# Kernel optimization log

Measured on AMD Instinct MI355X. Metric: run time of the kernel, lower is better.

Reference implementation:

```python
import jax, jax.numpy as jnp
import numpy as np
from jax import lax

B, T_IN, T_OUT = 32, 256, 500
N_MEL, ENC_DIM = 80, 512
ATT_RNN, DEC_RNN, PRENET, ATT_DIM = 1024, 1024, 256, 128
LOC_F, LOC_K = 32, 31
P_ATT_DROP, P_DEC_DROP = 0.1, 0.1


def setup_inputs() -> dict:
    key = jax.random.key(0)
    ks = jax.random.split(key, 24)
    rn = lambda k, s, sc=0.02: jax.random.normal(k, s, dtype=jnp.float32) * sc
    inp = {}
    inp['memory'] = jax.random.normal(ks[0], (B, T_IN, ENC_DIM), dtype=jnp.float32)
    inp['decoder_inputs'] = jax.random.normal(ks[1], (B, N_MEL, T_OUT), dtype=jnp.float32)
    inp['memory_lengths'] = jax.random.randint(ks[2], (B,), T_IN // 2, T_IN + 1)
    inp['prenet_w1'] = rn(ks[3], (PRENET, N_MEL))
    inp['prenet_w2'] = rn(ks[4], (PRENET, PRENET))
    inp['att_w_ih'] = rn(ks[5], (4 * ATT_RNN, PRENET + ENC_DIM))
    inp['att_w_hh'] = rn(ks[6], (4 * ATT_RNN, ATT_RNN))
    inp['att_b_ih'] = jnp.zeros((4 * ATT_RNN,), jnp.float32)
    inp['att_b_hh'] = jnp.zeros((4 * ATT_RNN,), jnp.float32)
    inp['query_w'] = rn(ks[7], (ATT_DIM, ATT_RNN))
    inp['memory_w'] = rn(ks[8], (ATT_DIM, ENC_DIM))
    inp['v_w'] = rn(ks[9], (1, ATT_DIM))
    inp['loc_conv_w'] = rn(ks[10], (LOC_F, 2, LOC_K))
    inp['loc_dense_w'] = rn(ks[11], (ATT_DIM, LOC_F))
    inp['dec_w_ih'] = rn(ks[12], (4 * DEC_RNN, ATT_RNN + ENC_DIM))
    inp['dec_w_hh'] = rn(ks[13], (4 * DEC_RNN, DEC_RNN))
    inp['dec_b_ih'] = jnp.zeros((4 * DEC_RNN,), jnp.float32)
    inp['dec_b_hh'] = jnp.zeros((4 * DEC_RNN,), jnp.float32)
    inp['proj_w'] = rn(ks[14], (N_MEL, DEC_RNN + ENC_DIM))
    inp['proj_b'] = jnp.zeros((N_MEL,), jnp.float32)
    inp['gate_w'] = rn(ks[15], (1, DEC_RNN + ENC_DIM))
    inp['gate_b'] = jnp.zeros((1,), jnp.float32)
    return inp


def _lstm_cell(x, h, c, w_ih, w_hh, b_ih, b_hh):
    gates = x @ w_ih.T + b_ih + h @ w_hh.T + b_hh
    i, f, g, o = jnp.split(gates, 4, axis=-1)
    c2 = jax.nn.sigmoid(f) * c + jax.nn.sigmoid(i) * jnp.tanh(g)
    h2 = jax.nn.sigmoid(o) * jnp.tanh(c2)
    return h2, c2


def _dropout_masks():
    # deterministic dropout masks (training=True semantics), keep-prob scaled
    kd = jax.random.key(1)
    k1, k2, k3, k4 = jax.random.split(kd, 4)
    m1 = jax.random.bernoulli(k1, 0.5, (T_OUT + 1, B, PRENET)).astype(jnp.float32) / 0.5
    m2 = jax.random.bernoulli(k2, 0.5, (T_OUT + 1, B, PRENET)).astype(jnp.float32) / 0.5
    ma = jax.random.bernoulli(k3, 1 - P_ATT_DROP, (T_OUT, B, ATT_RNN)).astype(jnp.float32) / (1 - P_ATT_DROP)
    md = jax.random.bernoulli(k4, 1 - P_DEC_DROP, (T_OUT, B, DEC_RNN)).astype(jnp.float32) / (1 - P_DEC_DROP)
    return m1, m2, ma, md


def _decode(memory, decoder_inputs, memory_lengths, prenet_w1, prenet_w2,
            att_w_ih, att_w_hh, att_b_ih, att_b_hh, query_w, memory_w, v_w,
            loc_conv_w, loc_dense_w, dec_w_ih, dec_w_hh, dec_b_ih, dec_b_hh,
            proj_w, proj_b, gate_w, gate_b):
    pm1, pm2, att_drop, dec_drop = _dropout_masks()
    processed_memory = jnp.einsum('bte,ae->bta', memory, memory_w)  # (B,T_in,128)
    pad_mask = jnp.arange(T_IN)[None, :] >= memory_lengths[:, None]  # True = padded

    # teacher-forced decoder inputs: (B,n_mel,T) -> (T,B,n_mel), prepend go frame
    dec_in = jnp.transpose(decoder_inputs, (2, 0, 1))
    dec_in = jnp.concatenate([jnp.zeros((1, B, N_MEL), dec_in.dtype), dec_in], 0)
    # prenet (relu + dropout p=0.5, always training)
    x = jax.nn.relu(dec_in @ prenet_w1.T) * pm1
    x = jax.nn.relu(x @ prenet_w2.T) * pm2
    prenet_out = x[:T_OUT]  # (T,B,256)

    pad = (LOC_K - 1) // 2

    def attention(att_h, aw, aw_cum):
        pq = att_h @ query_w.T  # (B,128)
        awc = jnp.stack([aw, aw_cum], axis=1)  # (B,2,T_in)
        loc = lax.conv_general_dilated(awc, loc_conv_w, (1,), [(pad, pad)],
                                       dimension_numbers=('NCH', 'OIH', 'NCH'))  # (B,32,T_in)
        loc = jnp.einsum('bft,af->bta', loc, loc_dense_w)  # (B,T_in,128)
        energies = jnp.tanh(pq[:, None, :] + loc + processed_memory) @ v_w[0]  # (B,T_in)
        energies = jnp.where(pad_mask, -jnp.inf, energies)
        w = jax.nn.softmax(energies, axis=1)
        ctx = jnp.einsum('bt,bte->be', w, memory)  # (B,512)
        return ctx, w

    def step(carry, xs):
        ah, ac, dh, dc, aw, aw_cum, ctx = carry
        pn, adm, ddm = xs
        cell_in = jnp.concatenate([pn, ctx], axis=-1)  # (B,768)
        ah, ac = _lstm_cell(cell_in, ah, ac, att_w_ih, att_w_hh, att_b_ih, att_b_hh)
        ah = ah * adm
        ctx, aw = attention(ah, aw, aw_cum)
        aw_cum = aw_cum + aw
        din = jnp.concatenate([ah, ctx], axis=-1)  # (B,1536)
        dh, dc = _lstm_cell(din, dh, dc, dec_w_ih, dec_w_hh, dec_b_ih, dec_b_hh)
        dh = dh * ddm
        dhac = jnp.concatenate([dh, ctx], axis=-1)  # (B,1536)
        mel = dhac @ proj_w.T + proj_b  # (B,80)
        gate = (dhac @ gate_w.T + gate_b)[:, 0]  # (B,)
        return (ah, ac, dh, dc, aw, aw_cum, ctx), (mel, gate, aw)

    z = lambda d: jnp.zeros((B, d), jnp.float32)
    init = (z(ATT_RNN), z(ATT_RNN), z(DEC_RNN), z(DEC_RNN),
            jnp.zeros((B, T_IN), jnp.float32), jnp.zeros((B, T_IN), jnp.float32), z(ENC_DIM))
    _, (mels, gates, aligns) = lax.scan(step, init, (prenet_out, att_drop, dec_drop))

    mel_outputs = jnp.transpose(mels, (1, 2, 0))   # (B, n_mel, T_out)
    gate_outputs = gates.T                          # (B, T_out)
    alignments = jnp.transpose(aligns, (1, 0, 2))   # (B, T_out, T_in)
    return mel_outputs, gate_outputs, alignments


def reference(memory, decoder_inputs, memory_lengths, prenet_w1, prenet_w2,
              att_w_ih, att_w_hh, att_b_ih, att_b_hh, query_w, memory_w, v_w,
              loc_conv_w, loc_dense_w, dec_w_ih, dec_w_hh, dec_b_ih, dec_b_hh,
              proj_w, proj_b, gate_w, gate_b):
    return _decode(memory, decoder_inputs, memory_lengths, prenet_w1, prenet_w2,
                   att_w_ih, att_w_hh, att_b_ih, att_b_hh, query_w, memory_w, v_w,
                   loc_conv_w, loc_dense_w, dec_w_ih, dec_w_hh, dec_b_ih, dec_b_hh,
                   proj_w, proj_b, gate_w, gate_b)
```

## Files before the change

kernel.cpp:

```cpp
#include <hip/hip_runtime.h>
#include <math.h>
#include <string.h>

#define TOUT 500
#define AOFF 1296000
#define GOFF 1280000
#define TF_BITS_XOR 1

typedef float f32x4 __attribute__((ext_vector_type(4)));
typedef short bf16x8 __attribute__((ext_vector_type(8)));
typedef unsigned short ushort4_t __attribute__((ext_vector_type(4)));
typedef unsigned u32x4 __attribute__((ext_vector_type(4)));

struct Params {
  const float *memory, *dec_in, *pw1, *pw2, *awih, *awhh, *abih, *abhh;
  const float *qw, *mw, *vw, *lcw, *ldw, *dwih, *dwhh, *dbih, *dbhh;
  const float *pjw, *pjb, *gw, *gb;
  const int* mlen;
  float* out;
  unsigned short *ahb0, *ahb1, *dhb0, *dhb1, *ctxb0, *ctxb1;
  unsigned *barcl;
  unsigned *barcr;
  unsigned *barg;
  float *x1, *w1t, *w2t, *mwt, *ldwt, *ba, *bd;
  unsigned short *pre_bf, *pm_bf, *mem_bf, *qw_bf, *wpa, *wpd;
  unsigned *mma, *mmd, *mm1, *mm2;
};

__host__ __device__ inline void tf_block(unsigned k0, unsigned k1, unsigned x0, unsigned x1,
                                         unsigned& o0, unsigned& o1) {
  unsigned ks2 = k0 ^ k1 ^ 0x1BD11BDAu;
  x0 += k0; x1 += k1;
#define TFR(r) { x0 += x1; x1 = (x1 << r) | (x1 >> (32 - r)); x1 ^= x0; }
  TFR(13) TFR(15) TFR(26) TFR(6)
  x0 += k1;  x1 += ks2 + 1u;
  TFR(17) TFR(29) TFR(16) TFR(24)
  x0 += ks2; x1 += k0 + 2u;
  TFR(13) TFR(15) TFR(26) TFR(6)
  x0 += k0;  x1 += k1 + 3u;
  TFR(17) TFR(29) TFR(16) TFR(24)
  x0 += k1;  x1 += ks2 + 4u;
  TFR(13) TFR(15) TFR(26) TFR(6)
  x0 += ks2; x1 += k0 + 5u;
#undef TFR
  o0 = x0; o1 = x1;
}

__device__ inline float sigf(float x) { return 1.f / (1.f + __expf(-x)); }
__device__ inline float tanh_fast(float x) {
  float ax = fabsf(x);
  float t = __expf(-2.f * ax);
  float r = (1.f - t) / (1.f + t);
  return copysignf(r, x);
}
__device__ inline unsigned short f2bf(float f) {
  unsigned u = __float_as_uint(f);
  unsigned r = (u + 0x7FFFu + ((u >> 16) & 1u)) >> 16;
  return (unsigned short)r;
}
__device__ inline float bf2f(unsigned short u) {
  return __uint_as_float((unsigned)u << 16);
}

__device__ inline unsigned long long ld_coh64(const void* ptr) {
  return __hip_atomic_load((unsigned long long*)ptr, __ATOMIC_RELAXED, __HIP_MEMORY_SCOPE_SYSTEM);
}
__device__ inline void st_coh32(unsigned* ptr, unsigned v) {
  __hip_atomic_store(ptr, v, __ATOMIC_RELAXED, __HIP_MEMORY_SCOPE_SYSTEM);
}

template<bool COH>
__device__ __forceinline__ u32x4 ld16(const void* ptr) {
  u32x4 r;
  if constexpr (COH)
    asm volatile("global_load_dwordx4 %0, %1, off sc0 sc1" : "=v"(r) : "v"(ptr));
  else
    asm volatile("global_load_dwordx4 %0, %1, off" : "=v"(r) : "v"(ptr));
  return r;
}

#define LD4(p) (*(const float4*)(p))

__global__ void maskgen_kernel(Params p, unsigned k1a, unsigned k1b, unsigned k2a, unsigned k2b,
                               unsigned k3a, unsigned k3b, unsigned k4a, unsigned k4b) {
  int t = blockIdx.x * 256 + threadIdx.x;
  unsigned ka, kb; unsigned* dst; float pp;
  if (t < 512000)       { ka = k3a; kb = k3b; dst = p.mma; pp = 0.9f; }
  else if (t < 1024000) { t -= 512000;  ka = k4a; kb = k4b; dst = p.mmd; pp = 0.9f; }
  else if (t < 1152256) { t -= 1024000; ka = k1a; kb = k1b; dst = p.mm1; pp = 0.5f; }
  else if (t < 1280512) { t -= 1152256; ka = k2a; kb = k2b; dst = p.mm2; pp = 0.5f; }
  else return;
  unsigned word = 0u;
  for (int i = 0; i < 32; ++i) {
    unsigned o0, o1;
    tf_block(ka, kb, 0u, (unsigned)t * 32u + (unsigned)i, o0, o1);
#if TF_BITS_XOR
    unsigned bits = o0 ^ o1;
#else
    unsigned bits = o0;
#endif
    unsigned fb = (bits >> 9) | 0x3f800000u;
    float u = __uint_as_float(fb) - 1.0f;
    if (u < pp) word |= (1u << i);
  }
  dst[t] = word;
}

__global__ void prep_misc(Params p) {
  int i = blockIdx.x * 256 + threadIdx.x;
  if (i < 20480) { int k = i >> 8, u = i & 255; p.w1t[i] = p.pw1[u * 80 + k]; return; }
  i -= 20480;
  if (i < 65536) { int k = i >> 8, u = i & 255; p.w2t[i] = p.pw2[u * 256 + k]; return; }
  i -= 65536;
  if (i < 65536) { int k = i >> 7, a = i & 127; p.mwt[i] = p.mw[a * 512 + k]; return; }
  i -= 65536;
  if (i < 131072) { p.qw_bf[i] = f2bf(p.qw[i]); return; }
  i -= 131072;
  if (i < 4096) { int f = i >> 7, a = i & 127; p.ldwt[i] = p.ldw[a * 32 + f]; return; }
  i -= 4096;
  if (i < 4096) { int col = (i & 3) * 1024 + (i >> 2); p.ba[i] = p.abih[col] + p.abhh[col]; return; }
  i -= 4096;
  if (i < 4096) { int col = (i & 3) * 1024 + (i >> 2); p.bd[i] = p.dbih[col] + p.dbhh[col]; return; }
  i -= 4096;
  if (i < 4194304) { p.mem_bf[i] = f2bf(p.memory[i]); return; }
}

__global__ void pack_att(Params p) {
  int idx = blockIdx.x * 256 + threadIdx.x;
  if (idx >= 256 * 56 * 64) return;
  int l = idx & 63;
  int c = (idx >> 6) % 56;
  int T = idx / (56 * 64);
  int n = T * 16 + (l & 15);
  int col = (n & 3) * 1024 + (n >> 2);
  int kb = c * 32 + 8 * (l >> 4);
  bf16x8 v;
#pragma unroll
  for (int j = 0; j < 8; ++j) {
    int k = kb + j;
    float f = (k < 768) ? p.awih[(size_t)col * 768 + k] : p.awhh[(size_t)col * 1024 + k - 768];
    v[j] = (short)f2bf(f);
  }
  *(bf16x8*)(p.wpa + (size_t)idx * 8) = v;
}
__global__ void pack_dec(Params p) {
  int idx = blockIdx.x * 256 + threadIdx.x;
  if (idx >= 256 * 80 * 64) return;
  int l = idx & 63;
  int c = (idx >> 6) % 80;
  int T = idx / (80 * 64);
  int n = T * 16 + (l & 15);
  int col = (n & 3) * 1024 + (n >> 2);
  int kb = c * 32 + 8 * (l >> 4);
  bf16x8 v;
#pragma unroll
  for (int j = 0; j < 8; ++j) {
    int k = kb + j;
    float f = (k < 1536) ? p.dwih[(size_t)col * 1536 + k] : p.dwhh[(size_t)col * 1024 + k - 1536];
    v[j] = (short)f2bf(f);
  }
  *(bf16x8*)(p.wpd + (size_t)idx * 8) = v;
}

__global__ void prenet1_kernel(Params p) {
  __shared__ float din[8][80];
  int wg = blockIdx.x, tid = threadIdx.x;
  int r0 = wg * 8;
  for (int idx = tid; idx < 8 * 80; idx += 256) {
    int j = idx / 80, kk = idx % 80;
    int r = r0 + j; int t = r >> 5, b = r & 31;
    din[j][kk] = (t == 0) ? 0.f : p.dec_in[(size_t)b * 40000 + (size_t)kk * 500 + (t - 1)];
  }
  __syncthreads();
  float acc[8] = {0,0,0,0,0,0,0,0};
  for (int k = 0; k < 80; ++k) {
    float wv = p.w1t[k * 256 + tid];
#pragma unroll
    for (int j = 0; j < 8; ++j) acc[j] += din[j][k] * wv;
  }
  for (int j = 0; j < 8; ++j) {
    int r = r0 + j;
    unsigned e = (unsigned)r * 256u + tid;
    float mv = ((p.mm1[e >> 5] >> (e & 31)) & 1u) ? 2.0f : 0.0f;
    p.x1[(size_t)r * 256 + tid] = fmaxf(acc[j], 0.f) * mv;
  }
}
__global__ void prenet2_kernel(Params p) {
  __shared__ float rows[8][256];
  int wg = blockIdx.x, tid = threadIdx.x;
  int r0 = wg * 8;
  for (int idx = tid; idx < 8 * 256; idx += 256) {
    int j = idx >> 8, kk = idx & 255;
    rows[j][kk] = p.x1[(size_t)(r0 + j) * 256 + kk];
  }
  __syncthreads();
  float acc[8] = {0,0,0,0,0,0,0,0};
  for (int k = 0; k < 256; ++k) {
    float wv = p.w2t[k * 256 + tid];
#pragma unroll
    for (int j = 0; j < 8; ++j) acc[j] += rows[j][k] * wv;
  }
  for (int j = 0; j < 8; ++j) {
    int r = r0 + j;
    unsigned e = (unsigned)r * 256u + tid;
    float mv = ((p.mm2[e >> 5] >> (e & 31)) & 1u) ? 2.0f : 0.0f;
    p.pre_bf[(size_t)r * 256 + tid] = f2bf(fmaxf(acc[j], 0.f) * mv);
  }
}

__global__ void pm_kernel(Params p) {
  __shared__ float mrows[16][512];
  int wg = blockIdx.x;
  int b = wg >> 4, tc = wg & 15;
  int tid = threadIdx.x;
  int t0 = tc * 16;
  for (int idx = tid; idx < 16 * 512; idx += 128) {
    int i = idx >> 9, k = idx & 511;
    mrows[i][k] = p.memory[((size_t)b * 256 + t0 + i) * 512 + k];
  }
  __syncthreads();
  float acc[16];
#pragma unroll
  for (int i = 0; i < 16; ++i) acc[i] = 0.f;
  for (int k = 0; k < 512; ++k) {
    float wv = p.mwt[k * 128 + tid];
#pragma unroll
    for (int i = 0; i < 16; ++i) acc[i] += mrows[i][k] * wv;
  }
  for (int i = 0; i < 16; ++i)
    p.pm_bf[((size_t)b * 256 + t0 + i) * 128 + tid] = f2bf(acc[i]);
}

template<int LEN, bool COH>
struct Seg {
  static constexpr int CPR = LEN / 8;
  static constexpr int N = (32 * CPR) / 512;
  u32x4 r[N];
  __device__ __forceinline__ void load(const unsigned short* src, int srcStride, int tid) {
#pragma unroll
    for (int i = 0; i < N; ++i) {
      int idx = tid + i * 512;
      int b = idx / CPR, c = idx % CPR;
      r[i] = ld16<COH>(src + (size_t)b * srcStride + c * 8);
    }
  }
  __device__ __forceinline__ void store(unsigned short* dst, int dstOff, int dstStride, int tid) {
#pragma unroll
    for (int i = 0; i < N; ++i) {
      int idx = tid + i * 512;
      int b = idx / CPR, c = idx % CPR;
      *(u32x4*)(dst + b * dstStride + dstOff + c * 8) = r[i];
    }
  }
};

__device__ __forceinline__ void drain_vm() {
  asm volatile("s_waitcnt vmcnt(0)" ::: "memory");
  __builtin_amdgcn_sched_barrier(0);
}

#define MFMA_BF16(a, b, c) __builtin_amdgcn_mfma_f32_16x16x32_bf16(a, b, c, 0, 0, 0)

template<int NC, int CPW, int P0J, bool ATT>
__device__ __forceinline__ void gemm_tile2(const Params& p, const bf16x8* bfa, const bf16x8* bfb,
                                           int lane, int v, int s,
                                           const unsigned short* ctxb_prev,
                                           const unsigned short* ahb_prev,
                                           const unsigned short* dhb_prev2,
                                           unsigned short* Abuf, float* pl, int tid) {
  const int arow = lane & 15;
  const int kgrp = (lane >> 4) * 8;
  f32x4 acc00 = {0,0,0,0}, acc01 = {0,0,0,0}, acc10 = {0,0,0,0}, acc11 = {0,0,0,0};

  const int RS0 = ATT ? 776 : 1288;
  if (ATT) {
    Seg<256, false> s0; Seg<512, true> s1;
    s0.load(p.pre_bf + (size_t)s * 32 * 256, 256, tid);
    s1.load(ctxb_prev, 512, tid);
    drain_vm();
    s0.store(Abuf, 0, RS0, tid);
    s1.store(Abuf, 256, RS0, tid);
  } else {
    Seg<1024, true> s0; Seg<256, true> s1;
    s0.load(ahb_prev, 1024, tid);
    s1.load(ctxb_prev, 512, tid);
    drain_vm();
    s0.store(Abuf, 0, RS0, tid);
    s1.store(Abuf, 1024, RS0, tid);
  }
  __syncthreads();
#pragma unroll
  for (int j = 0; j < P0J; ++j) {
    const int kc = (v + 8 * j) * 32;
    const int off = arow * RS0 + kc + kgrp;
    bf16x8 a0 = *(const bf16x8*)&Abuf[off];
    bf16x8 a1 = *(const bf16x8*)&Abuf[off + 16 * RS0];
    acc00 = MFMA_BF16(a0, bfa[j], acc00);
    acc01 = MFMA_BF16(a1, bfa[j], acc01);
    acc10 = MFMA_BF16(a0, bfb[j], acc10);
    acc11 = MFMA_BF16(a1, bfb[j], acc11);
  }
  __syncthreads();

  const int RS1 = ATT ? 1032 : 1288;
  if (ATT) {
    Seg<1024, true> s0;
    s0.load(ahb_prev, 1024, tid);
    drain_vm();
    s0.store(Abuf, 0, RS1, tid);
  } else {
    Seg<256, true> s0; Seg<1024, true> s1;
    s0.load(ctxb_prev + 256, 512, tid);
    s1.load(dhb_prev2, 1024, tid);
    drain_vm();
    s0.store(Abuf, 0, RS1, tid);
    s1.store(Abuf, 256, RS1, tid);
  }
  __syncthreads();
  const int K1 = ATT ? 768 : 1280;
#pragma unroll
  for (int j = P0J; j < CPW; ++j) {
    const int kc = (v + 8 * j) * 32 - K1;
    const int off = arow * RS1 + kc + kgrp;
    bf16x8 a0 = *(const bf16x8*)&Abuf[off];
    bf16x8 a1 = *(const bf16x8*)&Abuf[off + 16 * RS1];
    acc00 = MFMA_BF16(a0, bfa[j], acc00);
    acc01 = MFMA_BF16(a1, bfa[j], acc01);
    acc10 = MFMA_BF16(a0, bfb[j], acc10);
    acc11 = MFMA_BF16(a1, bfb[j], acc11);
  }
  __syncthreads();

  const int po = (lane & 15) * 17 + (lane >> 4) * 4;
#pragma unroll
  for (int j = 0; j < 4; ++j) {
    pl[v * 1088 +   0 + po + j] = acc00[j];
    pl[v * 1088 + 272 + po + j] = acc01[j];
    pl[v * 1088 + 544 + po + j] = acc10[j];
    pl[v * 1088 + 816 + po + j] = acc11[j];
  }
}

template<bool IS_ATT>
__device__ __forceinline__ void run_scan(const Params& p, int wg, int tid,
                                         unsigned short* Abuf, float* pl, float* gates,
                                         float* cst, float* aw_l, float* awc_l, float* sm,
                                         unsigned short* ahst, unsigned short* cxst,
                                         unsigned short* hst) {
  const int lane = tid & 63;
  const int v = tid >> 6;
  constexpr int NC  = IS_ATT ? 56 : 80;
  constexpr int CPW = IS_ATT ? 7 : 10;
  constexpr int P0J = IS_ATT ? 3 : 5;
  const int wgl = IS_ATT ? wg : (wg - 128);
  const int Tb  = wgl * 2;
  const int grp = wg >> 5;
  const int pollIdx = (wg & 7) * 32;

  bf16x8 bfa[CPW], bfb[CPW];
  {
    const unsigned short* wp = IS_ATT ? p.wpa : p.wpd;
#pragma unroll
    for (int j = 0; j < CPW; ++j) {
      const int c = v + 8 * j;
      const unsigned short* bp = wp + ((size_t)(Tb * NC + c) * 64 + lane) * 8;
      bfa[j] = *(const bf16x8*)bp;
      bfb[j] = *(const bf16x8*)(bp + (size_t)NC * 64 * 8);
    }
  }

  unsigned bargen = 0;
  auto gbar = [&]() {
    ++bargen;
    __syncthreads();
    if (tid == 0) {
      const int pr = bargen & 1;
      unsigned old = __hip_atomic_fetch_add(p.barcl + (pr * 8 + grp) * 32, 1u,
                                            __ATOMIC_RELAXED, __HIP_MEMORY_SCOPE_SYSTEM);
      bool done = false;
      if (old == 31u) {
        unsigned old2 = __hip_atomic_fetch_add(p.barcr + pr * 32, 1u,
                                               __ATOMIC_RELAXED, __HIP_MEMORY_SCOPE_SYSTEM);
        if (old2 == 7u) {
#pragma unroll
          for (int i = 0; i < 8; ++i)
            __hip_atomic_store(p.barcl + (pr * 8 + i) * 32, 0u, __ATOMIC_RELAXED, __HIP_MEMORY_SCOPE_SYSTEM);
          __hip_atomic_store(p.barcr + pr * 32, 0u, __ATOMIC_RELAXED, __HIP_MEMORY_SCOPE_SYSTEM);
          asm volatile("s_waitcnt vmcnt(0)" ::: "memory");
#pragma unroll
          for (int i = 0; i < 8; ++i)
            __hip_atomic_store(p.barg + i * 32, bargen, __ATOMIC_RELAXED, __HIP_MEMORY_SCOPE_SYSTEM);
          done = true;
        }
      }
      if (!done) {
        while (__hip_atomic_load(p.barg + pollIdx, __ATOMIC_RELAXED, __HIP_MEMORY_SCOPE_SYSTEM) < bargen)
          __builtin_amdgcn_s_sleep(2);
      }
    }
    __syncthreads();
  };

  for (int s = 0; s <= 500; ++s) {
    const int sb = s & 1;
    const unsigned short* ahb_prev  = sb ? p.ahb0 : p.ahb1;
    unsigned short*       ahb_cur   = sb ? p.ahb1 : p.ahb0;
    const unsigned short* dhb_prev2 = sb ? p.dhb1 : p.dhb0;
    unsigned short*       dhb_out   = sb ? p.dhb0 : p.dhb1;
    const unsigned short* ctxb_prev = sb ? p.ctxb0 : p.ctxb1;
    unsigned short*       ctxb_cur  = sb ? p.ctxb1 : p.ctxb0;

    const bool gemm_on = IS_ATT ? (s < 500) : (s >= 1);

    if (gemm_on)
      gemm_tile2<NC, CPW, P0J, IS_ATT>(p, bfa, bfb, lane, v, s, ctxb_prev, ahb_prev, dhb_prev2, Abuf, pl, tid);
    __syncthreads();
    if (gemm_on) {
      const float* bias = IS_ATT ? p.ba : p.bd;
      const int nb32 = wgl * 32;
#pragma unroll
      for (int rep = 0; rep < 2; ++rep) {
        int o = rep * 512 + tid;
        int tile = o >> 9, half = (o >> 8) & 1, n = (o >> 4) & 15, brow = o & 15;
        int o2 = (tile * 2 + half) * 272 + n * 17 + brow;
        float acc = 0.f;
#pragma unroll
        for (int w = 0; w < 8; ++w) acc += pl[w * 1088 + o2];
        int n_local = tile * 16 + n;
        gates[n_local * 33 + half * 16 + brow] = acc + bias[nb32 + n_local];
      }
    }
    __syncthreads();
    if (gemm_on && tid < 256) {
      int u_local = tid >> 5, b = tid & 31;
      float gi = gates[(u_local * 4 + 0) * 33 + b];
      float gf = gates[(u_local * 4 + 1) * 33 + b];
      float gg = gates[(u_local * 4 + 2) * 33 + b];
      float go = gates[(u_local * 4 + 3) * 33 + b];
      float I = sigf(gi), F = sigf(gf), G = tanh_fast(gg), O = sigf(go);
      float c2 = F * cst[tid] + I * G;
      float h = O * tanh_fast(c2);
      cst[tid] = c2;
      int u = wgl * 8 + u_local;
      float mv;
      if (IS_ATT) {
        unsigned e = ((unsigned)s * 32 + b) * 1024u + u;
        mv = ((p.mma[e >> 5] >> (e & 31)) & 1u) ? (1.f / 0.9f) : 0.f;
      } else {
        unsigned e = ((unsigned)(s - 1) * 32 + b) * 1024u + u;
        mv = ((p.mmd[e >> 5] >> (e & 31)) & 1u) ? (1.f / 0.9f) : 0.f;
      }
      hst[tid] = f2bf(h * mv);
    }
    __syncthreads();
    if (gemm_on && tid < 128) {
      int j = tid >> 5, bb = tid & 31;
      unsigned lo = hst[j * 64 + bb], hi = hst[j * 64 + 32 + bb];
      unsigned val = lo | (hi << 16);
      unsigned short* basep = IS_ATT ? ahb_cur : dhb_out;
      int T8 = wgl * 8;
      st_coh32((unsigned*)(basep + (size_t)bb * 1024 + T8 + 2 * j), val);
    }

    gbar();

    if (IS_ATT && wg < 32) {
      if (s < 500) {
        const int b = wg;
        unsigned short* locT_bf = (unsigned short*)pl;
        float* ldwt_l = (float*)((char*)(void*)pl + 16640);
        {
          const float4* srcw = (const float4*)p.ldwt;
          float4* dstw = (float4*)ldwt_l;
          dstw[tid] = srcw[tid];
          dstw[tid + 512] = srcw[tid + 512];
        }
        if (tid < 256) {
          unsigned long long q = ld_coh64((const unsigned long long*)(ahb_cur + (size_t)b * 1024) + tid);
          *(unsigned long long*)&ahst[tid * 4] = q;
        }
#pragma unroll
        for (int rep = 0; rep < 4; ++rep) {
          int qd = rep * 512 + tid;
          int f = qd >> 6, tq = (qd & 63) * 4;
          const float* wf = p.lcw + f * 62;
          float w[36]; float acc[4] = {0, 0, 0, 0};
#pragma unroll
          for (int j2 = 0; j2 < 9; ++j2) {
            float4 x = *(const float4*)&aw_l[tq + j2 * 4];
            w[j2*4] = x.x; w[j2*4+1] = x.y; w[j2*4+2] = x.z; w[j2*4+3] = x.w;
          }
#pragma unroll
          for (int k = 0; k < 31; ++k) {
            float cc = wf[k];
            acc[0] += w[k+1]*cc; acc[1] += w[k+2]*cc; acc[2] += w[k+3]*cc; acc[3] += w[k+4]*cc;
          }
#pragma unroll
          for (int j2 = 0; j2 < 9; ++j2) {
            float4 x = *(const float4*)&awc_l[tq + j2 * 4];
            w[j2*4] = x.x; w[j2*4+1] = x.y; w[j2*4+2] = x.z; w[j2*4+3] = x.w;
          }
#pragma unroll
          for (int k = 0; k < 31; ++k) {
            float cc = wf[31 + k];
            acc[0] += w[k+1]*cc; acc[1] += w[k+2]*cc; acc[2] += w[k+3]*cc; acc[3] += w[k+4]*cc;
          }
#pragma unroll
          for (int j2 = 0; j2 < 4; ++j2) locT_bf[f * 260 + tq + j2] = f2bf(acc[j2]);
        }
        __syncthreads();
        {
          int a = tid & 127, kq = tid >> 7;
          const unsigned short* qp = p.qw_bf + (size_t)a * 1024 + kq * 256;
          float acc = 0.f;
#pragma unroll 4
          for (int j = 0; j < 256; j += 8) {
            bf16x8 qv = *(const bf16x8*)(qp + j);
            bf16x8 av = *(const bf16x8*)&ahst[kq * 256 + j];
#pragma unroll
            for (int j2 = 0; j2 < 8; ++j2)
              acc += bf2f((unsigned short)av[j2]) * bf2f((unsigned short)qv[j2]);
          }
          sm[256 + kq * 128 + a] = acc;
          if (tid < 128) sm[128 + tid] = p.vw[tid];
        }
        __syncthreads();
        if (tid < 128) sm[tid] = sm[256 + tid] + sm[384 + tid] + sm[512 + tid] + sm[640 + tid];
        __syncthreads();
        {
          int t = tid & 255, h2 = tid >> 8;
          float lt[32];
#pragma unroll
          for (int f = 0; f < 32; ++f) lt[f] = bf2f(locT_bf[f * 260 + t]);
          const unsigned short* pmp = p.pm_bf + ((size_t)b * 256 + t) * 128;
          float e = 0.f;
#pragma unroll 2
          for (int ac = 0; ac < 16; ++ac) {
            int a0 = h2 * 64 + ac * 4;
            float4 l2 = {0, 0, 0, 0};
#pragma unroll
            for (int f = 0; f < 32; ++f) {
              float4 wv = *(const float4*)&ldwt_l[f * 128 + a0];
              l2.x += lt[f]*wv.x; l2.y += lt[f]*wv.y; l2.z += lt[f]*wv.z; l2.w += lt[f]*wv.w;
            }
            ushort4_t pv = *(const ushort4_t*)(pmp + a0);
            e += tanh_fast(sm[a0+0] + l2.x + bf2f(pv.x)) * sm[128+a0+0];
            e += tanh_fast(sm[a0+1] + l2.y + bf2f(pv.y)) * sm[128+a0+1];
            e += tanh_fast(sm[a0+2] + l2.z + bf2f(pv.z)) * sm[128+a0+2];
            e += tanh_fast(sm[a0+3] + l2.w + bf2f(pv.w)) * sm[128+a0+3];
          }
          sm[256 + h2 * 256 + t] = e;
        }
        __syncthreads();
        if (tid < 256) {
          float en = sm[256 + tid] + sm[512 + tid];
          float w = (tid < p.mlen[b]) ? __expf(en) : 0.f;
          sm[768 + tid] = w;
        }
        __syncthreads();
        if (tid < 32) {
          float sub = 0.f;
#pragma unroll
          for (int i = 0; i < 8; ++i) sub += sm[768 + tid * 8 + i];
          sm[256 + tid] = sub;
        }
        __syncthreads();
        if (tid == 0) {
          float S = 0.f;
#pragma unroll
          for (int i = 0; i < 32; ++i) S += sm[256 + i];
          sm[1281] = 1.f / S;
        }
        __syncthreads();
        if (tid < 256) {
          float awv = sm[768 + tid] * sm[1281];
          aw_l[16 + tid] = awv;
          awc_l[16 + tid] += awv;
          p.out[(size_t)AOFF + (size_t)b * 128000 + (size_t)s * 256 + tid] = awv;
          sm[1024 + tid] = awv;
        }
        __syncthreads();
        {
          const unsigned short* mb = p.mem_bf + (size_t)b * 131072 + tid;
          float acc = 0.f;
#pragma unroll 8
          for (int t2 = 0; t2 < 256; ++t2) acc += sm[1024 + t2] * bf2f(mb[(size_t)t2 * 512]);
          cxst[tid] = f2bf(acc);
        }
        __syncthreads();
        if (tid < 256) {
          unsigned val = (unsigned)cxst[2 * tid] | ((unsigned)cxst[2 * tid + 1] << 16);
          st_coh32((unsigned*)(ctxb_cur + (size_t)b * 512 + 2 * tid), val);
        }
      }
    } else if (wg >= 32) {
      if (s >= 1) {
        int idx = wg - 32;
        int b = idx / 7, c7 = idx % 7;
        int m0 = c7 * 12, mc = (c7 == 6) ? 8 : 12;
        if (tid < 384) {
          unsigned long long q;
          if (tid < 256) q = ld_coh64((const unsigned long long*)(dhb_out + (size_t)b * 1024) + tid);
          else           q = ld_coh64((const unsigned long long*)(ctxb_prev + (size_t)b * 512) + (tid - 256));
          *(unsigned long long*)&ahst[tid * 4] = q;
        }
        __syncthreads();
        int mi = tid >> 5, kg = tid & 31;
        if (mi < mc) {
          int m = m0 + mi;
          const float* pw = p.pjw + (size_t)m * 1536 + kg * 48;
          float acc = 0.f;
#pragma unroll 4
          for (int j = 0; j < 48; ++j) acc += bf2f(ahst[kg * 48 + j]) * pw[j];
          sm[mi * 32 + kg] = acc;
        }
        if (c7 == 6 && tid >= 384) {
          int kg2 = tid - 384;
          const float* gwp = p.gw + kg2 * 12;
          float acc = 0.f;
#pragma unroll
          for (int j = 0; j < 12; ++j) acc += bf2f(ahst[kg2 * 12 + j]) * gwp[j];
          sm[512 + kg2] = acc;
        }
        __syncthreads();
        if (tid < mc) {
          float r = p.pjb[m0 + tid];
#pragma unroll
          for (int j = 0; j < 32; ++j) r += sm[tid * 32 + j];
          p.out[(size_t)b * 40000 + (size_t)(m0 + tid) * 500 + (s - 1)] = r;
        }
        if (c7 == 6 && tid == 384) {
          float r = p.gb[0];
#pragma unroll
          for (int j = 0; j < 128; ++j) r += sm[512 + j];
          p.out[(size_t)GOFF + (size_t)b * 500 + (s - 1)] = r;
        }
      }
    }

    gbar();
  }
}

__global__ void __launch_bounds__(512, 2) scan_kernel(Params p) {
  const int wg = blockIdx.x;
  const int tid = threadIdx.x;

  __shared__ __align__(16) unsigned short Abuf[32 * 1288];
  float* pl = (float*)Abuf;
  __shared__ float gates[32 * 33];
  __shared__ float cst[256];
  __shared__ float aw_l[292], awc_l[292];
  __shared__ float sm[1536];
  __shared__ unsigned short ahst[1536];
  __shared__ unsigned short cxst[512];
  __shared__ unsigned short hst[256];

  if (tid < 256) cst[tid] = 0.f;
  if (tid < 292) { aw_l[tid] = 0.f; awc_l[tid] = 0.f; }

  if (wg < 128) run_scan<true >(p, wg, tid, Abuf, pl, gates, cst, aw_l, awc_l, sm, ahst, cxst, hst);
  else          run_scan<false>(p, wg, tid, Abuf, pl, gates, cst, aw_l, awc_l, sm, ahst, cxst, hst);
}

extern "C" void kernel_launch(void* const* d_in, const int* in_sizes, int n_in,
                              void* d_out, int out_size, void* d_ws, size_t ws_size,
                              hipStream_t stream) {
  Params p;
  p.memory = (const float*)d_in[0];
  p.dec_in = (const float*)d_in[1];
  p.mlen   = (const int*)d_in[2];
  p.pw1  = (const float*)d_in[3];
  p.pw2  = (const float*)d_in[4];
  p.awih = (const float*)d_in[5];
  p.awhh = (const float*)d_in[6];
  p.abih = (const float*)d_in[7];
  p.abhh = (const float*)d_in[8];
  p.qw   = (const float*)d_in[9];
  p.mw   = (const float*)d_in[10];
  p.vw   = (const float*)d_in[11];
  p.lcw  = (const float*)d_in[12];
  p.ldw  = (const float*)d_in[13];
  p.dwih = (const float*)d_in[14];
  p.dwhh = (const float*)d_in[15];
  p.dbih = (const float*)d_in[16];
  p.dbhh = (const float*)d_in[17];
  p.pjw  = (const float*)d_in[18];
  p.pjb  = (const float*)d_in[19];
  p.gw   = (const float*)d_in[20];
  p.gb   = (const float*)d_in[21];
  p.out  = (float*)d_out;

  char* cur = (char*)d_ws;
  auto allocf = [&](size_t n) { float* r = (float*)cur; cur += n * sizeof(float); return r; };
  auto allocs = [&](size_t n) { unsigned short* r = (unsigned short*)cur; cur += n * sizeof(unsigned short); return r; };
  p.ahb0 = allocs(32 * 1024); p.ahb1 = allocs(32 * 1024);
  p.dhb0 = allocs(32 * 1024); p.dhb1 = allocs(32 * 1024);
  p.ctxb0 = allocs(32 * 512); p.ctxb1 = allocs(32 * 512);
  p.barcl = (unsigned*)cur; cur += 2 * 8 * 32 * sizeof(unsigned);
  p.barcr = (unsigned*)cur; cur += 2 * 32 * sizeof(unsigned);
  p.barg  = (unsigned*)cur; cur += 8 * 32 * sizeof(unsigned);
  size_t state_bytes = (size_t)(cur - (char*)d_ws);
  p.x1   = allocf((size_t)500 * 32 * 256);
  p.w1t  = allocf(80 * 256);
  p.w2t  = allocf(256 * 256);
  p.mwt  = allocf(512 * 128);
  p.ldwt = allocf(32 * 128);
  p.ba   = allocf(4096);
  p.bd   = allocf(4096);
  p.pre_bf  = allocs((size_t)500 * 32 * 256);
  p.pm_bf   = allocs((size_t)32 * 256 * 128);
  p.mem_bf  = allocs((size_t)32 * 256 * 512);
  p.qw_bf   = allocs(128 * 1024);
  p.wpa     = allocs((size_t)256 * 56 * 64 * 8);
  p.wpd     = allocs((size_t)256 * 80 * 64 * 8);
  p.mma = (unsigned*)cur; cur += 512000u * 4;
  p.mmd = (unsigned*)cur; cur += 512000u * 4;
  p.mm1 = (unsigned*)cur; cur += 128256u * 4;
  p.mm2 = (unsigned*)cur; cur += 128256u * 4;

  (void)hipMemsetAsync(d_ws, 0, state_bytes, stream);

  unsigned k[8];
  {
    unsigned o0, o1;
    tf_block(0u, 1u, 0u, 0u, o0, o1); k[0] = o0; k[1] = o1;
    tf_block(0u, 1u, 0u, 1u, o0, o1); k[2] = o0; k[3] = o1;
    tf_block(0u, 1u, 0u, 2u, o0, o1); k[4] = o0; k[5] = o1;
    tf_block(0u, 1u, 0u, 3u, o0, o1); k[6] = o0; k[7] = o1;
  }

  maskgen_kernel<<<(1280512 + 255) / 256, 256, 0, stream>>>(p, k[0], k[1], k[2], k[3], k[4], k[5], k[6], k[7]);
  prep_misc<<<(4489216 + 255) / 256, 256, 0, stream>>>(p);
  pack_att<<<(917504 + 255) / 256, 256, 0, stream>>>(p);
  pack_dec<<<(1310720 + 255) / 256, 256, 0, stream>>>(p);
  prenet1_kernel<<<2000, 256, 0, stream>>>(p);
  prenet2_kernel<<<2000, 256, 0, stream>>>(p);
  pm_kernel<<<512, 128, 0, stream>>>(p);

  void* args[] = { (void*)&p };
  (void)hipLaunchCooperativeKernel((const void*)scan_kernel, dim3(256), dim3(512), args, 0, stream);
}
```

Baseline: 36.00 ms.

## Replace hierarchical atomic-counter grid barrier with per-block slot flags and master poller

```diff
diff --git a/kernel.cpp b/kernel.cpp
--- a/kernel.cpp
+++ b/kernel.cpp
@@ -19,9 +19,8 @@
   const int* mlen;
   float* out;
   unsigned short *ahb0, *ahb1, *dhb0, *dhb1, *ctxb0, *ctxb1;
-  unsigned *barcl;
-  unsigned *barcr;
-  unsigned *barg;
+  unsigned *slots;
+  unsigned *flags;
   float *x1, *w1t, *w2t, *mwt, *ldwt, *ba, *bd;
   unsigned short *pre_bf, *pm_bf, *mem_bf, *qw_bf, *wpa, *wpd;
   unsigned *mma, *mmd, *mm1, *mm2;
@@ -64,6 +63,9 @@
 
 __device__ inline unsigned long long ld_coh64(const void* ptr) {
   return __hip_atomic_load((unsigned long long*)ptr, __ATOMIC_RELAXED, __HIP_MEMORY_SCOPE_SYSTEM);
+}
+__device__ inline unsigned ld_coh32(const unsigned* ptr) {
+  return __hip_atomic_load(ptr, __ATOMIC_RELAXED, __HIP_MEMORY_SCOPE_SYSTEM);
 }
 __device__ inline void st_coh32(unsigned* ptr, unsigned v) {
   __hip_atomic_store(ptr, v, __ATOMIC_RELAXED, __HIP_MEMORY_SCOPE_SYSTEM);
@@ -341,7 +343,29 @@
   }
 }
 
-template<bool IS_ATT>
+template<bool MASTER>
+__device__ __forceinline__ void gbar(const Params& p, int wg, int tid, unsigned bargen) {
+  __syncthreads();
+  if (MASTER) {
+    if (tid == 0) st_coh32(p.slots + wg * 32, bargen);
+    for (;;) {
+      int ok = 1;
+      if (tid < 256) ok = (ld_coh32(p.slots + tid * 32) >= bargen) ? 1 : 0;
+      if (__syncthreads_count(ok) == 512) break;
+      __builtin_amdgcn_s_sleep(1);
+    }
+    if (tid < 8) st_coh32(p.flags + tid * 32, bargen);
+  } else {
+    if (tid == 0) {
+      st_coh32(p.slots + wg * 32, bargen);
+      while (ld_coh32(p.flags + (wg & 7) * 32) < bargen)
+        __builtin_amdgcn_s_sleep(2);
+    }
+    __syncthreads();
+  }
+}
+
+template<bool IS_ATT, bool MASTER>
 __device__ __forceinline__ void run_scan(const Params& p, int wg, int tid,
                                          unsigned short* Abuf, float* pl, float* gates,
                                          float* cst, float* aw_l, float* awc_l, float* sm,
@@ -354,8 +378,6 @@
   constexpr int P0J = IS_ATT ? 3 : 5;
   const int wgl = IS_ATT ? wg : (wg - 128);
   const int Tb  = wgl * 2;
-  const int grp = wg >> 5;
-  const int pollIdx = (wg & 7) * 32;
 
   bf16x8 bfa[CPW], bfb[CPW];
   {
@@ -370,36 +392,6 @@
   }
 
   unsigned bargen = 0;
-  auto gbar = [&]() {
-    ++bargen;
-    __syncthreads();
-    if (tid == 0) {
-      const int pr = bargen & 1;
-      unsigned old = __hip_atomic_fetch_add(p.barcl + (pr * 8 + grp) * 32, 1u,
-                                            __ATOMIC_RELAXED, __HIP_MEMORY_SCOPE_SYSTEM);
-      bool done = false;
-      if (old == 31u) {
-        unsigned old2 = __hip_atomic_fetch_add(p.barcr + pr * 32, 1u,
-                                               __ATOMIC_RELAXED, __HIP_MEMORY_SCOPE_SYSTEM);
-        if (old2 == 7u) {
-#pragma unroll
-          for (int i = 0; i < 8; ++i)
-            __hip_atomic_store(p.barcl + (pr * 8 + i) * 32, 0u, __ATOMIC_RELAXED, __HIP_MEMORY_SCOPE_SYSTEM);
-          __hip_atomic_store(p.barcr + pr * 32, 0u, __ATOMIC_RELAXED, __HIP_MEMORY_SCOPE_SYSTEM);
-          asm volatile("s_waitcnt vmcnt(0)" ::: "memory");
-#pragma unroll
-          for (int i = 0; i < 8; ++i)
-            __hip_atomic_store(p.barg + i * 32, bargen, __ATOMIC_RELAXED, __HIP_MEMORY_SCOPE_SYSTEM);
-          done = true;
-        }
-      }
-      if (!done) {
-        while (__hip_atomic_load(p.barg + pollIdx, __ATOMIC_RELAXED, __HIP_MEMORY_SCOPE_SYSTEM) < bargen)
-          __builtin_amdgcn_s_sleep(2);
-      }
-    }
-    __syncthreads();
-  };
 
   for (int s = 0; s <= 500; ++s) {
     const int sb = s & 1;
@@ -462,7 +454,7 @@
       st_coh32((unsigned*)(basep + (size_t)bb * 1024 + T8 + 2 * j), val);
     }
 
-    gbar();
+    gbar<MASTER>(p, wg, tid, ++bargen);
 
     if (IS_ATT && wg < 32) {
       if (s < 500) {
@@ -638,7 +630,7 @@
       }
     }
 
-    gbar();
+    gbar<MASTER>(p, wg, tid, ++bargen);
   }
 }
 
@@ -659,8 +651,12 @@
   if (tid < 256) cst[tid] = 0.f;
   if (tid < 292) { aw_l[tid] = 0.f; awc_l[tid] = 0.f; }
 
-  if (wg < 128) run_scan<true >(p, wg, tid, Abuf, pl, gates, cst, aw_l, awc_l, sm, ahst, cxst, hst);
-  else          run_scan<false>(p, wg, tid, Abuf, pl, gates, cst, aw_l, awc_l, sm, ahst, cxst, hst);
+  if (wg < 128) {
+    if (wg == 32) run_scan<true, true >(p, wg, tid, Abuf, pl, gates, cst, aw_l, awc_l, sm, ahst, cxst, hst);
+    else          run_scan<true, false>(p, wg, tid, Abuf, pl, gates, cst, aw_l, awc_l, sm, ahst, cxst, hst);
+  } else {
+    run_scan<false, false>(p, wg, tid, Abuf, pl, gates, cst, aw_l, awc_l, sm, ahst, cxst, hst);
+  }
 }
 
 extern "C" void kernel_launch(void* const* d_in, const int* in_sizes, int n_in,
@@ -697,9 +693,8 @@
   p.ahb0 = allocs(32 * 1024); p.ahb1 = allocs(32 * 1024);
   p.dhb0 = allocs(32 * 1024); p.dhb1 = allocs(32 * 1024);
   p.ctxb0 = allocs(32 * 512); p.ctxb1 = allocs(32 * 512);
-  p.barcl = (unsigned*)cur; cur += 2 * 8 * 32 * sizeof(unsigned);
-  p.barcr = (unsigned*)cur; cur += 2 * 32 * sizeof(unsigned);
-  p.barg  = (unsigned*)cur; cur += 8 * 32 * sizeof(unsigned);
+  p.slots = (unsigned*)cur; cur += 256 * 32 * sizeof(unsigned);
+  p.flags = (unsigned*)cur; cur += 8 * 32 * sizeof(unsigned);
   size_t state_bytes = (size_t)(cur - (char*)d_ws);
   p.x1   = allocf((size_t)500 * 32 * 256);
   p.w1t  = allocf(80 * 256);
```

After: 35.49 ms. No clear change (-1.4%).
